# Performance work log

Measured on AMD Instinct MI355X. Metric: run time of the kernel, lower is better.

Reference implementation:

```python
import jax, jax.numpy as jnp
import numpy as np
from jax import lax

B, H, W = 256, 26, 4
LAT, QOUT = 64, 1024
K, D, Z = 4, 32, 64   # num_flows, num_ortho_vecs, z_size
STEPS = 100
BN_EPS = 1e-5


def setup_inputs():
    ks = iter(jax.random.split(jax.random.key(0), 80))
    def rn(shape, s=0.05):
        return jax.random.normal(next(ks), shape, jnp.float32) * s
    z1 = lambda n: jnp.zeros((n,), jnp.float32)
    o1 = lambda n: jnp.ones((n,), jnp.float32)
    return {
        "x": jax.random.normal(next(ks), (B, 1, H, W), jnp.float32),
        "eps": jax.random.normal(next(ks), (B, LAT), jnp.float32),
        "cw1": rn((32, 1, 3, 4)), "cb1": z1(32), "g1": o1(32), "be1": z1(32),
        "cw2": rn((16, 32, 5, 1)), "cb2": z1(16), "g2": o1(16), "be2": z1(16),
        "cw3": rn((8, 16, 7, 1)), "cb3": z1(8), "g3": o1(8), "be3": z1(8),
        "d1_w": rn((112, QOUT)), "d1_b": z1(QOUT), "bn1_g": o1(QOUT), "bn1_b": z1(QOUT),
        "mu_w": rn((QOUT, LAT)), "mu_b": z1(LAT),
        "lv_w": rn((QOUT, LAT)), "lv_b": z1(LAT),
        "ad_w": rn((QOUT, K * D * D)), "ad_b": z1(K * D * D),
        "adg1_w": rn((QOUT, K * D)), "adg1_b": z1(K * D),
        "adg2_w": rn((QOUT, K * D)), "adg2_b": z1(K * D),
        "aq_w": rn((QOUT, K * Z * D)), "aq_b": rn((K * Z * D,), 0.05),
        "ab_w": rn((QOUT, K * D)), "ab_b": z1(K * D),
        "d3_w": rn((LAT, QOUT)), "d3_b": z1(QOUT), "bn3_g": o1(QOUT), "bn3_b": z1(QOUT),
        "d4_w": rn((QOUT, 112)), "d4_b": z1(112), "bn4_g": o1(112), "bn4_b": z1(112),
        "tw1": rn((8, 16, 7, 1)), "tb1": z1(16), "tg1": o1(16), "tbe1": z1(16),
        "tw2": rn((16, 32, 5, 1)), "tb2": z1(32), "tg2": o1(32), "tbe2": z1(32),
        "tw3": rn((32, 1, 3, 4)), "tb3": z1(1),
    }


def _conv(x, w, b):
    y = lax.conv_general_dilated(x, w, (1, 1), 'VALID',
                                 dimension_numbers=('NCHW', 'OIHW', 'NCHW'))
    return y + b[None, :, None, None]


def _tconv(x, w, b):
    # torch ConvTranspose2d weight layout (in, out, kH, kW) == OIHW of the
    # forward conv being transposed -> transpose_kernel=True matches torch.
    y = lax.conv_transpose(x, w, (1, 1), 'VALID',
                           dimension_numbers=('NCHW', 'OIHW', 'NCHW'),
                           transpose_kernel=True)
    return y + b[None, :, None, None]


def _bn2d(x, g, b):  # BatchNorm2d, training mode (biased batch stats)
    m = x.mean((0, 2, 3), keepdims=True)
    v = ((x - m) ** 2).mean((0, 2, 3), keepdims=True)
    return (x - m) * lax.rsqrt(v + BN_EPS) * g[None, :, None, None] + b[None, :, None, None]


def _bn1d(x, g, b):  # BatchNorm1d, training mode
    m = x.mean(0)
    v = ((x - m) ** 2).mean(0)
    return (x - m) * lax.rsqrt(v + BN_EPS) * g + b


def reference(x, eps, cw1, cb1, g1, be1, cw2, cb2, g2, be2, cw3, cb3, g3, be3,
              d1_w, d1_b, bn1_g, bn1_b, mu_w, mu_b, lv_w, lv_b,
              ad_w, ad_b, adg1_w, adg1_b, adg2_w, adg2_b, aq_w, aq_b, ab_w, ab_b,
              d3_w, d3_b, bn3_g, bn3_b, d4_w, d4_b, bn4_g, bn4_b,
              tw1, tb1, tg1, tbe1, tw2, tb2, tg2, tbe2, tw3, tb3):
    # ---- encoder CNN ----
    h = jax.nn.relu(_bn2d(_conv(x, cw1, cb1), g1, be1))
    h = jax.nn.relu(_bn2d(_conv(h, cw2, cb2), g2, be2))
    h = jax.nn.relu(_bn2d(_conv(h, cw3, cb3), g3, be3))   # (B,8,14,1)
    out = h.reshape(B, -1)                                 # (B,112)
    out = jax.nn.relu(_bn1d(out @ d1_w + d1_b, bn1_g, bn1_b))
    mean = out @ mu_w + mu_b
    logvar = out @ lv_w + lv_b
    # ---- amortized flow parameters ----
    full_d = (out @ ad_w + ad_b).reshape(B, D, D, K)
    diag1 = jnp.tanh(out @ adg1_w + adg1_b).reshape(B, D, K)
    diag2 = jnp.tanh(out @ adg2_w + adg2_b).reshape(B, D, K)
    triu = jnp.triu(jnp.ones((D, D), x.dtype), 1)[None, :, :, None]
    di = jnp.arange(D)
    r1 = (full_d * triu).at[:, di, di, :].set(diag1)
    r2 = (jnp.transpose(full_d, (0, 2, 1, 3)) * triu).at[:, di, di, :].set(diag2)
    q = out @ aq_w + aq_b                                  # (B, K*Z*D)
    bflow = (out @ ab_w + ab_b).reshape(B, 1, D, K)
    # ---- Bjorck orthogonalization (100 fixed-point steps) ----
    qn = q.reshape(B * K, Z * D)
    qn = qn / jnp.linalg.norm(qn, axis=1, keepdims=True)
    amat = qn.reshape(B * K, Z, D)
    eye = jnp.eye(D, dtype=x.dtype)
    @jax.checkpoint
    def step(a, _):
        gram = jnp.einsum('nzd,nze->nde', a, a)            # a^T a, (N,D,D)
        a = jnp.einsum('nzd,nde->nze', a, eye + 0.5 * (eye - gram))
        return a, None
    amat, _ = lax.scan(step, amat, None, length=STEPS)
    q_ortho = amat.reshape(B, K, Z, D).transpose(1, 0, 2, 3)  # (K,B,Z,D)
    # ---- reparameterize + Sylvester flows ----
    z0 = mean + eps * jnp.exp(0.5 * logvar)
    z = z0
    ldj = jnp.zeros((B,), x.dtype)
    for k in range(K):
        r1k, r2k, qk, bk = r1[..., k], r2[..., k], q_ortho[k], bflow[..., k]
        qr2 = jnp.einsum('bzd,bed->bze', qk, r2k)          # q @ r2^T (B,Z,D)
        qr1 = jnp.einsum('bzd,bde->bze', qk, r1k)          # q @ r1   (B,Z,D)
        r2qzb = jnp.einsum('bz,bzd->bd', z, qr2)[:, None, :] + bk  # (B,1,D)
        z = jnp.einsum('bod,bzd->boz', jnp.tanh(r2qzb), qr1)[:, 0, :] + z
        dr1 = r1k[:, di, di]
        dr2 = r2k[:, di, di]
        diag_j = (1.0 - jnp.tanh(r2qzb) ** 2)[:, 0, :] * (dr1 * dr2) + 1.0
        ldj = ldj + jnp.log(jnp.abs(diag_j)).sum(-1)
    # ---- decoder ----
    d = jax.nn.relu(_bn1d(z @ d3_w + d3_b, bn3_g, bn3_b))
    d = jax.nn.relu(_bn1d(d @ d4_w + d4_b, bn4_g, bn4_b))
    d = d.reshape(B, 8, 14, 1)
    d = jax.nn.relu(_bn2d(_tconv(d, tw1, tb1), tg1, tbe1))
    d = jax.nn.relu(_bn2d(_tconv(d, tw2, tb2), tg2, tbe2))
    x_dec = _tconv(d, tw3, tb3)
    return (x_dec, mean, logvar, ldj, z0, z)
```

## Files before the change

kernel.cpp:

```cpp
#include <hip/hip_runtime.h>
#include <math.h>

#define NS_STEPS 30

typedef __attribute__((ext_vector_type(8))) _Float16 half8;
typedef __attribute__((ext_vector_type(4))) _Float16 half4v;
typedef __attribute__((ext_vector_type(8))) short short8;
typedef __attribute__((ext_vector_type(4))) float floatx4;

static __device__ inline unsigned short f2bf(float f) {
  union { float f; unsigned u; } v; v.f = f;
  unsigned r = v.u + 0x7fffu + ((v.u >> 16) & 1u);
  return (unsigned short)(r >> 16);
}
static __device__ inline float bf2f(unsigned short h) {
  union { unsigned u; float f; } v; v.u = ((unsigned)h) << 16;
  return v.f;
}

__global__ __launch_bounds__(256) void conv1_k(const float* __restrict__ x,
    const float* __restrict__ w, const float* __restrict__ bias,
    float* __restrict__ out) {
  __shared__ float ws[384];
  int tid = threadIdx.x;
  for (int i = tid; i < 384; i += 256) ws[i] = w[i];
  __syncthreads();
  int idx = blockIdx.x * 256 + tid;
  if (idx >= 196608) return;
  int b = idx / 768, r = idx % 768;
  int c = r / 24, h = r % 24;
  const float* xb = x + b * 104 + h * 4;
  const float* wc = ws + c * 12;
  float acc = bias[c];
  #pragma unroll
  for (int kh = 0; kh < 3; kh++) {
    #pragma unroll
    for (int kw = 0; kw < 4; kw++)
      acc += xb[kh * 4 + kw] * wc[kh * 4 + kw];
  }
  out[idx] = acc;
}

__global__ __launch_bounds__(256) void conv2_k(const float* __restrict__ in,
    const float* __restrict__ w, const float* __restrict__ bias,
    float* __restrict__ out) {
  __shared__ float ws[2560];
  int tid = threadIdx.x;
  for (int i = tid; i < 2560; i += 256) ws[i] = w[i];
  __syncthreads();
  int idx = blockIdx.x * 256 + tid;
  if (idx >= 81920) return;
  int b = idx / 320, r = idx % 320;
  int c = r / 20, h = r % 20;
  const float* ib = in + b * 768 + h;
  const float* wc = ws + c * 160;
  float acc = bias[c];
  for (int i = 0; i < 32; i++) {
    #pragma unroll
    for (int kh = 0; kh < 5; kh++)
      acc += ib[i * 24 + kh] * wc[i * 5 + kh];
  }
  out[idx] = acc;
}

__global__ __launch_bounds__(256) void conv3_k(const float* __restrict__ in,
    const float* __restrict__ w, const float* __restrict__ bias,
    float* __restrict__ out) {
  __shared__ float ws[896];
  int tid = threadIdx.x;
  for (int i = tid; i < 896; i += 256) ws[i] = w[i];
  __syncthreads();
  int idx = blockIdx.x * 256 + tid;
  if (idx >= 28672) return;
  int b = idx / 112, r = idx % 112;
  int c = r / 14, h = r % 14;
  const float* ib = in + b * 320 + h;
  const float* wc = ws + c * 112;
  float acc = bias[c];
  for (int i = 0; i < 16; i++) {
    #pragma unroll
    for (int kh = 0; kh < 7; kh++)
      acc += ib[i * 20 + kh] * wc[i * 7 + kh];
  }
  out[idx] = acc;
}

__global__ __launch_bounds__(256) void tconv1_k(const float* __restrict__ in,
    const float* __restrict__ w, const float* __restrict__ bias,
    float* __restrict__ out) {
  __shared__ float ws[896];
  int tid = threadIdx.x;
  for (int i = tid; i < 896; i += 256) ws[i] = w[i];
  __syncthreads();
  int idx = blockIdx.x * 256 + tid;
  if (idx >= 81920) return;
  int b = idx / 320, r = idx % 320;
  int c = r / 20, s = r % 20;
  float acc = bias[c];
  for (int o = 0; o < 8; o++) {
    #pragma unroll
    for (int kh = 0; kh < 7; kh++) {
      int hs = s - kh;
      if (hs >= 0 && hs < 14)
        acc += in[b * 112 + o * 14 + hs] * ws[o * 112 + c * 7 + kh];
    }
  }
  out[idx] = acc;
}

__global__ __launch_bounds__(256) void tconv2_k(const float* __restrict__ in,
    const float* __restrict__ w, const float* __restrict__ bias,
    float* __restrict__ out) {
  __shared__ float ws[2560];
  int tid = threadIdx.x;
  for (int i = tid; i < 2560; i += 256) ws[i] = w[i];
  __syncthreads();
  int idx = blockIdx.x * 256 + tid;
  if (idx >= 196608) return;
  int b = idx / 768, r = idx % 768;
  int c = r / 24, s = r % 24;
  float acc = bias[c];
  for (int o = 0; o < 16; o++) {
    #pragma unroll
    for (int kh = 0; kh < 5; kh++) {
      int hs = s - kh;
      if (hs >= 0 && hs < 20)
        acc += in[b * 320 + o * 20 + hs] * ws[o * 160 + c * 5 + kh];
    }
  }
  out[idx] = acc;
}

__global__ __launch_bounds__(256) void tconv3_k(const float* __restrict__ in,
    const float* __restrict__ w, const float* __restrict__ bias,
    float* __restrict__ out) {
  __shared__ float ws[384];
  int tid = threadIdx.x;
  for (int i = tid; i < 384; i += 256) ws[i] = w[i];
  __syncthreads();
  int idx = blockIdx.x * 256 + tid;
  if (idx >= 26624) return;
  int b = idx / 104, r = idx % 104;
  int sh = r / 4, sw = r % 4;
  float acc = bias[0];
  for (int o = 0; o < 32; o++) {
    #pragma unroll
    for (int kh = 0; kh < 3; kh++) {
      int hs = sh - kh;
      if (hs >= 0 && hs < 24)
        acc += in[b * 768 + o * 24 + hs] * ws[o * 12 + kh * 4 + sw];
    }
  }
  out[idx] = acc;
}

__global__ __launch_bounds__(256) void bn2d_k(float* __restrict__ x,
    const float* __restrict__ g, const float* __restrict__ be,
    int C, int HW) {
  __shared__ float rs[256], rs2[256];
  int c = blockIdx.x, tid = threadIdx.x;
  int total = 256 * HW;
  float s = 0.f, s2 = 0.f;
  for (int i = tid; i < total; i += 256) {
    int b = i / HW, j = i - b * HW;
    float v = x[(b * C + c) * HW + j];
    s += v; s2 += v * v;
  }
  rs[tid] = s; rs2[tid] = s2;
  __syncthreads();
  for (int off = 128; off > 0; off >>= 1) {
    if (tid < off) { rs[tid] += rs[tid + off]; rs2[tid] += rs2[tid + off]; }
    __syncthreads();
  }
  float m = rs[0] / (float)total;
  float var = rs2[0] / (float)total - m * m;
  float rstd = rsqrtf(var + 1e-5f) * g[c];
  float bb = be[c];
  for (int i = tid; i < total; i += 256) {
    int b = i / HW, j = i - b * HW;
    size_t idx = (size_t)(b * C + c) * HW + j;
    float v = (x[idx] - m) * rstd + bb;
    x[idx] = v > 0.f ? v : 0.f;
  }
}

__global__ __launch_bounds__(256) void bn1d_k(float* __restrict__ x,
    const float* __restrict__ g, const float* __restrict__ be, int N) {
  __shared__ float p1[8][32], p2[8][32];
  int t = threadIdx.x;
  int cl = t & 31, rg = t >> 5;
  int c = blockIdx.x * 32 + cl;
  float s = 0.f, s2 = 0.f;
  if (c < N) {
    for (int r = rg * 32; r < rg * 32 + 32; r++) {
      float v = x[r * N + c];
      s += v; s2 += v * v;
    }
  }
  p1[rg][cl] = s; p2[rg][cl] = s2;
  __syncthreads();
  float ts = 0.f, ts2 = 0.f;
  #pragma unroll
  for (int i = 0; i < 8; i++) { ts += p1[i][cl]; ts2 += p2[i][cl]; }
  float m = ts * (1.f / 256.f);
  float var = ts2 * (1.f / 256.f) - m * m;
  float rstd = rsqrtf(var + 1e-5f) * ((c < N) ? g[c] : 1.f);
  float bb = (c < N) ? be[c] : 0.f;
  if (c < N) {
    for (int r = rg * 32; r < rg * 32 + 32; r++) {
      float v = (x[r * N + c] - m) * rstd + bb;
      x[r * N + c] = v > 0.f ? v : 0.f;
    }
  }
}

__global__ __launch_bounds__(256) void gemm_os_k(const float* __restrict__ A,
    const float* __restrict__ W, const float* __restrict__ bias,
    float* __restrict__ C, int K, int N) {
  __shared__ float As[112 * 68];
  __shared__ float Bs[112 * 68];
  int tid = threadIdx.x;
  int nb = blockIdx.x, mb = blockIdx.y;
  int K16 = K >> 4;
  {
    int row = tid >> 2;
    const float* Ar = A + (size_t)(mb * 64 + row) * K;
    for (int i = 0; i < K16; i++) {
      int j = (tid & 3) + 4 * i;
      float4 v = *(const float4*)(Ar + j * 4);
      int k = j * 4;
      As[k * 68 + row] = v.x;
      As[(k + 1) * 68 + row] = v.y;
      As[(k + 2) * 68 + row] = v.z;
      As[(k + 3) * 68 + row] = v.w;
    }
  }
  {
    int n4 = (tid & 15) * 4;
    for (int i = 0; i < K16; i++) {
      int k = (tid >> 4) + 16 * i;
      float4 v = *(const float4*)(W + (size_t)k * N + nb * 64 + n4);
      *(float4*)(Bs + k * 68 + n4) = v;
    }
  }
  __syncthreads();
  int tm = tid >> 4, tn = tid & 15;
  int m0 = tm * 4, n0 = tn * 4;
  float acc[4][4] = {{0.f}};
  #pragma unroll 8
  for (int kk = 0; kk < K; kk++) {
    float4 a = *(const float4*)(As + kk * 68 + m0);
    float4 b = *(const float4*)(Bs + kk * 68 + n0);
    acc[0][0] += a.x*b.x; acc[0][1] += a.x*b.y; acc[0][2] += a.x*b.z; acc[0][3] += a.x*b.w;
    acc[1][0] += a.y*b.x; acc[1][1] += a.y*b.y; acc[1][2] += a.y*b.z; acc[1][3] += a.y*b.w;
    acc[2][0] += a.z*b.x; acc[2][1] += a.z*b.y; acc[2][2] += a.z*b.z; acc[2][3] += a.z*b.w;
    acc[3][0] += a.w*b.x; acc[3][1] += a.w*b.y; acc[3][2] += a.w*b.z; acc[3][3] += a.w*b.w;
  }
  #pragma unroll
  for (int i = 0; i < 4; i++) {
    int m = mb * 64 + m0 + i;
    #pragma unroll
    for (int j = 0; j < 4; j++) {
      int n = nb * 64 + n0 + j;
      C[(size_t)m * N + n] = acc[i][j] + bias[n];
    }
  }
}

__global__ __launch_bounds__(256) void gemm_ks_k(const float* __restrict__ A,
    const float* __restrict__ W, const float* __restrict__ bias,
    float* __restrict__ C) {
  __shared__ float As[64 * 68];
  __shared__ float Bs[64 * 68];
  int tid = threadIdx.x;
  int nb = blockIdx.x, mb = blockIdx.y, kc = blockIdx.z;
  int k0 = kc * 64;
  {
    int row = tid >> 2;
    const float* Ar = A + (size_t)(mb * 64 + row) * 1024 + k0;
    #pragma unroll
    for (int i = 0; i < 4; i++) {
      int j = (tid & 3) + 4 * i;
      float4 v = *(const float4*)(Ar + j * 4);
      int k = j * 4;
      As[k * 68 + row] = v.x;
      As[(k + 1) * 68 + row] = v.y;
      As[(k + 2) * 68 + row] = v.z;
      As[(k + 3) * 68 + row] = v.w;
    }
  }
  {
    int n4 = (tid & 15) * 4;
    int nbase = nb * 64 + n4;
    #pragma unroll
    for (int i = 0; i < 4; i++) {
      int k = (tid >> 4) + 16 * i;
      const float* Wr = W + (size_t)(k0 + k) * 112;
      float4 v;
      v.x = (nbase     < 112) ? Wr[nbase]     : 0.f;
      v.y = (nbase + 1 < 112) ? Wr[nbase + 1] : 0.f;
      v.z = (nbase + 2 < 112) ? Wr[nbase + 2] : 0.f;
      v.w = (nbase + 3 < 112) ? Wr[nbase + 3] : 0.f;
      *(float4*)(Bs + k * 68 + n4) = v;
    }
  }
  __syncthreads();
  int tm = tid >> 4, tn = tid & 15;
  int m0 = tm * 4, n0 = tn * 4;
  float acc[4][4] = {{0.f}};
  #pragma unroll 8
  for (int kk = 0; kk < 64; kk++) {
    float4 a = *(const float4*)(As + kk * 68 + m0);
    float4 b = *(const float4*)(Bs + kk * 68 + n0);
    acc[0][0] += a.x*b.x; acc[0][1] += a.x*b.y; acc[0][2] += a.x*b.z; acc[0][3] += a.x*b.w;
    acc[1][0] += a.y*b.x; acc[1][1] += a.y*b.y; acc[1][2] += a.y*b.z; acc[1][3] += a.y*b.w;
    acc[2][0] += a.z*b.x; acc[2][1] += a.z*b.y; acc[2][2] += a.z*b.z; acc[2][3] += a.z*b.w;
    acc[3][0] += a.w*b.x; acc[3][1] += a.w*b.y; acc[3][2] += a.w*b.z; acc[3][3] += a.w*b.w;
  }
  #pragma unroll
  for (int i = 0; i < 4; i++) {
    int m = mb * 64 + m0 + i;
    #pragma unroll
    for (int j = 0; j < 4; j++) {
      int n = nb * 64 + n0 + j;
      if (n < 112) {
        float v = acc[i][j] + (kc == 0 ? bias[n] : 0.f);
        atomicAdd(&C[m * 112 + n], v);
      }
    }
  }
}

__global__ __launch_bounds__(256) void prep_a_k(const float* __restrict__ A,
    short* __restrict__ ahi, short* __restrict__ alo) {
  int gi = blockIdx.x * 256 + threadIdx.x;
  int lane = gi & 63;
  int t = gi >> 6;
  int mt = t & 3; t >>= 2;
  int c = t & 31; int mb = t >> 5;
  int row = mb * 64 + mt * 16 + (lane & 15);
  int k0 = c * 32 + (lane >> 4) * 8;
  const float* src = A + (size_t)row * 1024 + k0;
  float4 v0 = *(const float4*)(src);
  float4 v1 = *(const float4*)(src + 4);
  float av[8] = {v0.x, v0.y, v0.z, v0.w, v1.x, v1.y, v1.z, v1.w};
  short8 h, lo;
  #pragma unroll
  for (int i = 0; i < 8; i++) {
    unsigned short hh = f2bf(av[i]);
    h[i] = (short)hh;
    lo[i] = (short)f2bf(av[i] - bf2f(hh));
  }
  *(short8*)(ahi + (size_t)gi * 8) = h;
  *(short8*)(alo + (size_t)gi * 8) = lo;
}

struct HeadArgs {
  const float* W[7];
  const float* b[7];
  float* dst[7];
  int off[8];
  int ldw[7];
  int op[7];
};

__global__ __launch_bounds__(256) void heads_mfma_k(const short* __restrict__ ahi,
                                                    const short* __restrict__ alo,
                                                    HeadArgs ha) {
  __shared__ __align__(16) short Wsh[2][2][2048];
  int tid = threadIdx.x;
  int nb = blockIdx.x, mb = blockIdx.y;
  int r = 0;
  int gc = nb * 64;
  while (gc >= ha.off[r + 1]) r++;
  const float* Wp = ha.W[r];
  const float* bias = ha.b[r];
  float* dst = ha.dst[r];
  int ldw = ha.ldw[r];
  int op = ha.op[r];
  int nloc0 = gc - ha.off[r];

  int w = tid >> 6, l = tid & 63;
  int lane16 = l & 15, quad = l >> 4;

  int c64 = tid & 63, q4 = tid >> 6;
  const float* wcol = Wp + (size_t)q4 * 8 * ldw + nloc0 + c64;
  int wg = ((c64 >> 4) * 64 + q4 * 16 + (c64 & 15)) * 8;

  const short* agh = ahi + (size_t)mb * 65536;
  const short* agl = alo + (size_t)mb * 65536;

  const floatx4 zero4 = {0.f, 0.f, 0.f, 0.f};
  floatx4 acc[4] = {zero4, zero4, zero4, zero4};

  float wreg[8];
  short8 whi, wlo;

  #pragma unroll
  for (int j = 0; j < 8; j++) wreg[j] = wcol[(size_t)j * ldw];
  #pragma unroll
  for (int j = 0; j < 8; j++) {
    unsigned short hh = f2bf(wreg[j]);
    whi[j] = (short)hh;
    wlo[j] = (short)f2bf(wreg[j] - bf2f(hh));
  }
  *(short8*)(&Wsh[0][0][wg]) = whi;
  *(short8*)(&Wsh[0][1][wg]) = wlo;
  #pragma unroll
  for (int j = 0; j < 8; j++) wreg[j] = wcol[(size_t)(32 + j) * ldw];
  __syncthreads();
  #pragma unroll
  for (int j = 0; j < 8; j++) {
    unsigned short hh = f2bf(wreg[j]);
    whi[j] = (short)hh;
    wlo[j] = (short)f2bf(wreg[j] - bf2f(hh));
  }

  for (int ch = 0; ch < 32; ++ch) {
    int p = ch & 1;
    if (ch < 31) {
      *(short8*)(&Wsh[p ^ 1][0][wg]) = whi;
      *(short8*)(&Wsh[p ^ 1][1][wg]) = wlo;
    }
    if (ch < 30) {
      #pragma unroll
      for (int j = 0; j < 8; j++)
        wreg[j] = wcol[(size_t)((ch + 2) * 32 + j) * ldw];
    }
    short8 bh = *(const short8*)(&Wsh[p][0][(w * 64 + l) * 8]);
    short8 bl = *(const short8*)(&Wsh[p][1][(w * 64 + l) * 8]);
    short8 ah[4], al4[4];
    #pragma unroll
    for (int mt = 0; mt < 4; mt++) {
      size_t ao = (size_t)ch * 2048 + mt * 512 + l * 8;
      ah[mt]  = *(const short8*)(agh + ao);
      al4[mt] = *(const short8*)(agl + ao);
    }
    #pragma unroll
    for (int mt = 0; mt < 4; mt++) {
      acc[mt] = __builtin_amdgcn_mfma_f32_16x16x32_bf16(ah[mt], bh, acc[mt], 0, 0, 0);
      acc[mt] = __builtin_amdgcn_mfma_f32_16x16x32_bf16(ah[mt], bl, acc[mt], 0, 0, 0);
      acc[mt] = __builtin_amdgcn_mfma_f32_16x16x32_bf16(al4[mt], bh, acc[mt], 0, 0, 0);
    }
    if (ch < 30) {
      #pragma unroll
      for (int j = 0; j < 8; j++) {
        unsigned short hh = f2bf(wreg[j]);
        whi[j] = (short)hh;
        wlo[j] = (short)f2bf(wreg[j] - bf2f(hh));
      }
    }
    __syncthreads();
  }

  int n = nloc0 + w * 16 + lane16;
  float bv = bias[n];
  #pragma unroll
  for (int mt = 0; mt < 4; mt++) {
    #pragma unroll
    for (int i = 0; i < 4; i++) {
      int m = mb * 64 + mt * 16 + quad * 4 + i;
      float v = acc[mt][i] + bv;
      if (op == 1) v = tanhf(v);
      dst[(size_t)m * ldw + n] = v;
    }
  }
}

__global__ __launch_bounds__(64) void ns_f16split_k(const float* __restrict__ q,
                                                    float* __restrict__ amat) {
  __align__(16) __shared__ _Float16 arena[12288];
  int l = threadIdx.x;
  int lane16 = l & 15, quad = l >> 4;
  _Float16* Ah_cm = arena;
  _Float16* Al_cm = arena + 2304;
  _Float16* Mh_cm = arena + 4608;
  _Float16* Ml_cm = arena + 5888;
  _Float16* Ah_rm = arena + 7168;
  _Float16* Al_rm = arena + 9728;
  float* Afin = (float*)arena;

  const float* g = q + (size_t)blockIdx.x * 2048;
  float* o = amat + (size_t)blockIdx.x * 2048;

  float vals[32];
  float ss = 0.f;
  #pragma unroll
  for (int j = 0; j < 8; j++) {
    float4 v = *(const float4*)(g + l * 32 + j * 4);
    vals[4*j] = v.x; vals[4*j+1] = v.y; vals[4*j+2] = v.z; vals[4*j+3] = v.w;
    ss += v.x*v.x + v.y*v.y + v.z*v.z + v.w*v.w;
  }
  #pragma unroll
  for (int off = 32; off > 0; off >>= 1) ss += __shfl_xor(ss, off);
  float rn = rsqrtf(ss);
  #pragma unroll
  for (int i = 0; i < 32; i++) vals[i] *= rn;
  #pragma unroll
  for (int j = 0; j < 8; j++) {
    half4v ph, pl;
    #pragma unroll
    for (int r = 0; r < 4; r++) {
      float v = vals[4*j + r];
      _Float16 h = (_Float16)v;
      _Float16 lo = (_Float16)(v - (float)h);
      ph[r] = h; pl[r] = lo;
    }
    *(half4v*)(Ah_rm + l * 40 + j * 4) = ph;
    *(half4v*)(Al_rm + l * 40 + j * 4) = pl;
  }
  #pragma unroll
  for (int i = 0; i < 32; i++) {
    float v = vals[i];
    _Float16 h = (_Float16)v;
    Ah_cm[i * 72 + l] = h;
    Al_cm[i * 72 + l] = (_Float16)(v - (float)h);
  }
  __syncthreads();

  const floatx4 zero4 = {0.f, 0.f, 0.f, 0.f};
  for (int s = 0; s < NS_STEPS; s++) {
    bool last = (s == NS_STEPS - 1);
    half8 fah[2][2], fal[2][2];
    #pragma unroll
    for (int ti = 0; ti < 2; ti++)
      #pragma unroll
      for (int c = 0; c < 2; c++) {
        fah[ti][c] = *(half8*)(Ah_cm + (ti * 16 + lane16) * 72 + c * 32 + quad * 8);
        fal[ti][c] = *(half8*)(Al_cm + (ti * 16 + lane16) * 72 + c * 32 + quad * 8);
      }
    floatx4 gf[2][2] = {{zero4, zero4}, {zero4, zero4}};
    #pragma unroll
    for (int ti = 0; ti < 2; ti++)
      #pragma unroll
      for (int tj = 0; tj < 2; tj++)
        #pragma unroll
        for (int c = 0; c < 2; c++) {
          gf[ti][tj] = __builtin_amdgcn_mfma_f32_16x16x32_f16(
              fah[ti][c], fah[tj][c], gf[ti][tj], 0, 0, 0);
          gf[ti][tj] = __builtin_amdgcn_mfma_f32_16x16x32_f16(
              fah[ti][c], fal[tj][c], gf[ti][tj], 0, 0, 0);
          gf[ti][tj] = __builtin_amdgcn_mfma_f32_16x16x32_f16(
              fal[ti][c], fah[tj][c], gf[ti][tj], 0, 0, 0);
        }
    #pragma unroll
    for (int ti = 0; ti < 2; ti++)
      #pragma unroll
      for (int tj = 0; tj < 2; tj++) {
        int col = tj * 16 + lane16;
        int row0 = ti * 16 + quad * 4;
        half4v ph, pl;
        #pragma unroll
        for (int r = 0; r < 4; r++) {
          float m = ((row0 + r) == col ? 1.5f : 0.f) - 0.5f * gf[ti][tj][r];
          _Float16 h = (_Float16)m;
          ph[r] = h; pl[r] = (_Float16)(m - (float)h);
        }
        *(half4v*)(Mh_cm + col * 40 + row0) = ph;
        *(half4v*)(Ml_cm + col * 40 + row0) = pl;
      }
    __syncthreads();
    half8 fmh[2], fml[2], fbh[4], fbl[4];
    #pragma unroll
    for (int ti = 0; ti < 2; ti++) {
      fmh[ti] = *(half8*)(Mh_cm + (ti * 16 + lane16) * 40 + quad * 8);
      fml[ti] = *(half8*)(Ml_cm + (ti * 16 + lane16) * 40 + quad * 8);
    }
    #pragma unroll
    for (int tj = 0; tj < 4; tj++) {
      fbh[tj] = *(half8*)(Ah_rm + (tj * 16 + lane16) * 40 + quad * 8);
      fbl[tj] = *(half8*)(Al_rm + (tj * 16 + lane16) * 40 + quad * 8);
    }
    floatx4 df[2][4];
    #pragma unroll
    for (int ti = 0; ti < 2; ti++)
      #pragma unroll
      for (int tj = 0; tj < 4; tj++) {
        df[ti][tj] = __builtin_amdgcn_mfma_f32_16x16x32_f16(
            fmh[ti], fbh[tj], zero4, 0, 0, 0);
        df[ti][tj] = __builtin_amdgcn_mfma_f32_16x16x32_f16(
            fmh[ti], fbl[tj], df[ti][tj], 0, 0, 0);
        df[ti][tj] = __builtin_amdgcn_mfma_f32_16x16x32_f16(
            fml[ti], fbh[tj], df[ti][tj], 0, 0, 0);
      }
    __syncthreads();
    if (!last) {
      #pragma unroll
      for (int ti = 0; ti < 2; ti++)
        #pragma unroll
        for (int tj = 0; tj < 4; tj++) {
          int z = tj * 16 + lane16;
          int d0 = ti * 16 + quad * 4;
          half4v ph, pl;
          #pragma unroll
          for (int r = 0; r < 4; r++) {
            float v = df[ti][tj][r];
            _Float16 h = (_Float16)v;
            ph[r] = h; pl[r] = (_Float16)(v - (float)h);
          }
          *(half4v*)(Ah_rm + z * 40 + d0) = ph;
          *(half4v*)(Al_rm + z * 40 + d0) = pl;
          #pragma unroll
          for (int r = 0; r < 4; r++) {
            Ah_cm[(d0 + r) * 72 + z] = ph[r];
            Al_cm[(d0 + r) * 72 + z] = pl[r];
          }
        }
    } else {
      #pragma unroll
      for (int ti = 0; ti < 2; ti++)
        #pragma unroll
        for (int tj = 0; tj < 4; tj++) {
          int z = tj * 16 + lane16;
          int d0 = ti * 16 + quad * 4;
          float4 v;
          v.x = df[ti][tj][0]; v.y = df[ti][tj][1];
          v.z = df[ti][tj][2]; v.w = df[ti][tj][3];
          *(float4*)(Afin + z * 36 + d0) = v;
        }
    }
    __syncthreads();
  }
  #pragma unroll
  for (int j = 0; j < 8; j++) {
    int f = j * 256 + l * 4;
    int z = f >> 5, d = f & 31;
    float4 v = *(const float4*)(Afin + z * 36 + d);
    *(float4*)(o + f) = v;
  }
}

__global__ __launch_bounds__(64) void flow_k(const float* __restrict__ amat,
    const float* __restrict__ fd, const float* __restrict__ dg1,
    const float* __restrict__ dg2, const float* __restrict__ ab,
    const float* __restrict__ eps, float* __restrict__ dout) {
  __shared__ float Ps[32][64];
  __shared__ float wsh[32], tsh[32], ush[32];
  int b = blockIdx.x, l = threadIdx.x;
  float mv  = dout[26624 + b * 64 + l];
  float lvv = dout[43008 + b * 64 + l];
  float z0 = mv + eps[b * 64 + l] * expf(0.5f * lvv);
  dout[59648 + b * 64 + l] = z0;
  float zv = z0;
  float ldj = 0.f;
  float q[32];
  for (int k = 0; k < 4; k++) {
    const float4* qrow = (const float4*)(amat + (size_t)(b * 4 + k) * 2048 + l * 32);
    #pragma unroll
    for (int j = 0; j < 8; j++) {
      float4 v = qrow[j];
      q[4*j] = v.x; q[4*j+1] = v.y; q[4*j+2] = v.z; q[4*j+3] = v.w;
    }
    #pragma unroll
    for (int d = 0; d < 32; d++) Ps[d][l] = zv * q[d];
    __syncthreads();
    if (l < 32) {
      const float4* pr = (const float4*)Ps[l];
      float s = 0.f;
      #pragma unroll
      for (int j = 0; j < 16; j++) {
        float4 v = pr[j];
        s += v.x + v.y + v.z + v.w;
      }
      wsh[l] = s;
    }
    __syncthreads();
    if (l < 32) {
      int e = l;
      float acc = ab[b * 128 + e * 4 + k] + wsh[e] * dg2[b * 128 + e * 4 + k];
      for (int d = e + 1; d < 32; d++)
        acc += wsh[d] * fd[b * 4096 + d * 128 + e * 4 + k];
      float tt = tanhf(acc);
      tsh[e] = tt;
      float dd = (1.f - tt * tt) * (dg1[b*128 + e*4 + k] * dg2[b*128 + e*4 + k]) + 1.f;
      ldj += logf(fabsf(dd));
    }
    __syncthreads();
    if (l < 32) {
      int d = l;
      float acc = tsh[d] * dg1[b * 128 + d * 4 + k];
      for (int e = d + 1; e < 32; e++)
        acc += fd[b * 4096 + d * 128 + e * 4 + k] * tsh[e];
      ush[d] = acc;
    }
    __syncthreads();
    #pragma unroll
    for (int d = 0; d < 32; d++) zv += q[d] * ush[d];
    __syncthreads();
  }
  dout[76032 + b * 64 + l] = zv;
  for (int off = 16; off > 0; off >>= 1) ldj += __shfl_down(ldj, off, 32);
  if (l == 0) dout[59392 + b] = ldj;
}

extern "C" void kernel_launch(void* const* d_in, const int* in_sizes, int n_in,
                              void* d_out, int out_size, void* d_ws, size_t ws_size,
                              hipStream_t stream) {
  (void)in_sizes; (void)n_in; (void)out_size; (void)ws_size;
  const float* x     = (const float*)d_in[0];
  const float* eps   = (const float*)d_in[1];
  const float* cw1   = (const float*)d_in[2];
  const float* cb1   = (const float*)d_in[3];
  const float* g1    = (const float*)d_in[4];
  const float* be1   = (const float*)d_in[5];
  const float* cw2   = (const float*)d_in[6];
  const float* cb2   = (const float*)d_in[7];
  const float* g2    = (const float*)d_in[8];
  const float* be2   = (const float*)d_in[9];
  const float* cw3   = (const float*)d_in[10];
  const float* cb3   = (const float*)d_in[11];
  const float* g3    = (const float*)d_in[12];
  const float* be3   = (const float*)d_in[13];
  const float* d1_w  = (const float*)d_in[14];
  const float* d1_b  = (const float*)d_in[15];
  const float* bn1_g = (const float*)d_in[16];
  const float* bn1_b = (const float*)d_in[17];
  const float* mu_w  = (const float*)d_in[18];
  const float* mu_b  = (const float*)d_in[19];
  const float* lv_w  = (const float*)d_in[20];
  const float* lv_b  = (const float*)d_in[21];
  const float* ad_w  = (const float*)d_in[22];
  const float* ad_b  = (const float*)d_in[23];
  const float* adg1_w= (const float*)d_in[24];
  const float* adg1_b= (const float*)d_in[25];
  const float* adg2_w= (const float*)d_in[26];
  const float* adg2_b= (const float*)d_in[27];
  const float* aq_w  = (const float*)d_in[28];
  const float* aq_b  = (const float*)d_in[29];
  const float* ab_w  = (const float*)d_in[30];
  const float* ab_b  = (const float*)d_in[31];
  const float* d3_w  = (const float*)d_in[32];
  const float* d3_b  = (const float*)d_in[33];
  const float* bn3_g = (const float*)d_in[34];
  const float* bn3_b = (const float*)d_in[35];
  const float* d4_w  = (const float*)d_in[36];
  const float* d4_b  = (const float*)d_in[37];
  const float* bn4_g = (const float*)d_in[38];
  const float* bn4_b = (const float*)d_in[39];
  const float* tw1   = (const float*)d_in[40];
  const float* tb1   = (const float*)d_in[41];
  const float* tg1   = (const float*)d_in[42];
  const float* tbe1  = (const float*)d_in[43];
  const float* tw2   = (const float*)d_in[44];
  const float* tb2   = (const float*)d_in[45];
  const float* tg2   = (const float*)d_in[46];
  const float* tbe2  = (const float*)d_in[47];
  const float* tw3   = (const float*)d_in[48];
  const float* tb3   = (const float*)d_in[49];

  float* out = (float*)d_out;
  float* wsf = (float*)d_ws;
  float* h1   = wsf;
  float* h2   = wsf + 196608;
  float* h3   = wsf + 278528;
  float* out1 = wsf + 307200;
  float* fd   = wsf + 569344;
  float* dg1  = wsf + 1617920;
  float* dg2  = wsf + 1650688;
  float* qb   = wsf + 1683456;
  float* ab   = wsf + 3780608;
  float* amat = wsf + 3813376;
  float* dec1 = out1;
  float* dec2 = h3;
  float* t1   = h2;
  float* t2   = h1;

  short* ahi = (short*)wsf;
  short* alo = ahi + 262144;

  float* mean_o = out + 26624;
  float* lv_o   = out + 43008;
  float* z_o    = out + 76032;

  conv1_k<<<768, 256, 0, stream>>>(x, cw1, cb1, h1);
  bn2d_k<<<32, 256, 0, stream>>>(h1, g1, be1, 32, 24);
  conv2_k<<<320, 256, 0, stream>>>(h1, cw2, cb2, h2);
  bn2d_k<<<16, 256, 0, stream>>>(h2, g2, be2, 16, 20);
  conv3_k<<<112, 256, 0, stream>>>(h2, cw3, cb3, h3);
  bn2d_k<<<8, 256, 0, stream>>>(h3, g3, be3, 8, 14);

  gemm_os_k<<<dim3(16, 4), 256, 0, stream>>>(h3, d1_w, d1_b, out1, 112, 1024);
  bn1d_k<<<32, 256, 0, stream>>>(out1, bn1_g, bn1_b, 1024);

  prep_a_k<<<128, 256, 0, stream>>>(out1, ahi, alo);

  HeadArgs ha;
  ha.W[0] = mu_w;   ha.b[0] = mu_b;   ha.dst[0] = mean_o; ha.ldw[0] = 64;   ha.op[0] = 0;
  ha.W[1] = lv_w;   ha.b[1] = lv_b;   ha.dst[1] = lv_o;   ha.ldw[1] = 64;   ha.op[1] = 0;
  ha.W[2] = ad_w;   ha.b[2] = ad_b;   ha.dst[2] = fd;     ha.ldw[2] = 4096; ha.op[2] = 0;
  ha.W[3] = adg1_w; ha.b[3] = adg1_b; ha.dst[3] = dg1;    ha.ldw[3] = 128;  ha.op[3] = 1;
  ha.W[4] = adg2_w; ha.b[4] = adg2_b; ha.dst[4] = dg2;    ha.ldw[4] = 128;  ha.op[4] = 1;
  ha.W[5] = aq_w;   ha.b[5] = aq_b;   ha.dst[5] = qb;     ha.ldw[5] = 8192; ha.op[5] = 0;
  ha.W[6] = ab_w;   ha.b[6] = ab_b;   ha.dst[6] = ab;     ha.ldw[6] = 128;  ha.op[6] = 0;
  ha.off[0] = 0;    ha.off[1] = 64;   ha.off[2] = 128;  ha.off[3] = 4224;
  ha.off[4] = 4352; ha.off[5] = 4480; ha.off[6] = 12672; ha.off[7] = 12800;
  heads_mfma_k<<<dim3(200, 4), 256, 0, stream>>>(ahi, alo, ha);

  ns_f16split_k<<<1024, 64, 0, stream>>>(qb, amat);
  flow_k<<<256, 64, 0, stream>>>(amat, fd, dg1, dg2, ab, eps, out);

  gemm_os_k<<<dim3(16, 4), 256, 0, stream>>>(z_o, d3_w, d3_b, dec1, 64, 1024);
  bn1d_k<<<32, 256, 0, stream>>>(dec1, bn3_g, bn3_b, 1024);
  hipMemsetAsync(dec2, 0, 28672 * sizeof(float), stream);
  gemm_ks_k<<<dim3(2, 4, 16), 256, 0, stream>>>(dec1, d4_w, d4_b, dec2);
  bn1d_k<<<4, 256, 0, stream>>>(dec2, bn4_g, bn4_b, 112);

  tconv1_k<<<320, 256, 0, stream>>>(dec2, tw1, tb1, t1);
  bn2d_k<<<16, 256, 0, stream>>>(t1, tg1, tbe1, 16, 20);
  tconv2_k<<<768, 256, 0, stream>>>(t1, tw2, tb2, t2);
  bn2d_k<<<32, 256, 0, stream>>>(t2, tg2, tbe2, 32, 24);
  tconv3_k<<<104, 256, 0, stream>>>(t2, tw3, tb3, out);
}
```

Measured before the change: 521.2 us.

## Retile heads GEMM so each block covers all rows and reuses weight tiles

The heads GEMM grid drops the M-dimension blocks, so each 64-column block now computes all 256 rows, with each wave owning 64 rows and all four 16-column N fragments. Each weight chunk is converted to bf16 hi/lo and staged in LDS once per column block rather than four times, and A-fragments are register double-buffered one chunk ahead. The aim is to cut the redundant weight loads and conversions, which are the main global traffic. In exchange the grid shrinks from 800 to 200 blocks and each thread holds 16 accumulators plus prefetch buffers, which lowers occupancy and may leave CUs idle.

```diff
diff --git a/kernel.cpp b/kernel.cpp
--- a/kernel.cpp
+++ b/kernel.cpp
@@ -369,7 +369,7 @@
                                                     HeadArgs ha) {
   __shared__ __align__(16) short Wsh[2][2][2048];
   int tid = threadIdx.x;
-  int nb = blockIdx.x, mb = blockIdx.y;
+  int nb = blockIdx.x;
   int r = 0;
   int gc = nb * 64;
   while (gc >= ha.off[r + 1]) r++;
@@ -387,14 +387,19 @@
   const float* wcol = Wp + (size_t)q4 * 8 * ldw + nloc0 + c64;
   int wg = ((c64 >> 4) * 64 + q4 * 16 + (c64 & 15)) * 8;
 
-  const short* agh = ahi + (size_t)mb * 65536;
-  const short* agl = alo + (size_t)mb * 65536;
+  const short* agh = ahi + (size_t)w * 65536;
+  const short* agl = alo + (size_t)w * 65536;
 
   const floatx4 zero4 = {0.f, 0.f, 0.f, 0.f};
-  floatx4 acc[4] = {zero4, zero4, zero4, zero4};
+  floatx4 acc[4][4];
+  #pragma unroll
+  for (int mt = 0; mt < 4; mt++)
+    #pragma unroll
+    for (int nf = 0; nf < 4; nf++) acc[mt][nf] = zero4;
 
   float wreg[8];
   short8 whi, wlo;
+  short8 aCh[4], aCl[4], aNh[4], aNl[4];
 
   #pragma unroll
   for (int j = 0; j < 8; j++) wreg[j] = wcol[(size_t)j * ldw];
@@ -408,6 +413,12 @@
   *(short8*)(&Wsh[0][1][wg]) = wlo;
   #pragma unroll
   for (int j = 0; j < 8; j++) wreg[j] = wcol[(size_t)(32 + j) * ldw];
+  #pragma unroll
+  for (int mt = 0; mt < 4; mt++) {
+    size_t ao = (size_t)mt * 512 + l * 8;
+    aCh[mt] = *(const short8*)(agh + ao);
+    aCl[mt] = *(const short8*)(agl + ao);
+  }
   __syncthreads();
   #pragma unroll
   for (int j = 0; j < 8; j++) {
@@ -416,6 +427,7 @@
     wlo[j] = (short)f2bf(wreg[j] - bf2f(hh));
   }
 
+  #pragma unroll 2
   for (int ch = 0; ch < 32; ++ch) {
     int p = ch & 1;
     if (ch < 31) {
@@ -427,21 +439,28 @@
       for (int j = 0; j < 8; j++)
         wreg[j] = wcol[(size_t)((ch + 2) * 32 + j) * ldw];
     }
-    short8 bh = *(const short8*)(&Wsh[p][0][(w * 64 + l) * 8]);
-    short8 bl = *(const short8*)(&Wsh[p][1][(w * 64 + l) * 8]);
-    short8 ah[4], al4[4];
-    #pragma unroll
-    for (int mt = 0; mt < 4; mt++) {
-      size_t ao = (size_t)ch * 2048 + mt * 512 + l * 8;
-      ah[mt]  = *(const short8*)(agh + ao);
-      al4[mt] = *(const short8*)(agl + ao);
-    }
-    #pragma unroll
-    for (int mt = 0; mt < 4; mt++) {
-      acc[mt] = __builtin_amdgcn_mfma_f32_16x16x32_bf16(ah[mt], bh, acc[mt], 0, 0, 0);
-      acc[mt] = __builtin_amdgcn_mfma_f32_16x16x32_bf16(ah[mt], bl, acc[mt], 0, 0, 0);
-      acc[mt] = __builtin_amdgcn_mfma_f32_16x16x32_bf16(al4[mt], bh, acc[mt], 0, 0, 0);
-    }
+    if (ch < 31) {
+      #pragma unroll
+      for (int mt = 0; mt < 4; mt++) {
+        size_t ao = (size_t)((ch + 1) * 4 + mt) * 512 + l * 8;
+        aNh[mt] = *(const short8*)(agh + ao);
+        aNl[mt] = *(const short8*)(agl + ao);
+      }
+    }
+    short8 bh[4], bl[4];
+    #pragma unroll
+    for (int nf = 0; nf < 4; nf++) {
+      bh[nf] = *(const short8*)(&Wsh[p][0][(nf * 64 + l) * 8]);
+      bl[nf] = *(const short8*)(&Wsh[p][1][(nf * 64 + l) * 8]);
+    }
+    #pragma unroll
+    for (int mt = 0; mt < 4; mt++)
+      #pragma unroll
+      for (int nf = 0; nf < 4; nf++) {
+        acc[mt][nf] = __builtin_amdgcn_mfma_f32_16x16x32_bf16(aCh[mt], bh[nf], acc[mt][nf], 0, 0, 0);
+        acc[mt][nf] = __builtin_amdgcn_mfma_f32_16x16x32_bf16(aCh[mt], bl[nf], acc[mt][nf], 0, 0, 0);
+        acc[mt][nf] = __builtin_amdgcn_mfma_f32_16x16x32_bf16(aCl[mt], bh[nf], acc[mt][nf], 0, 0, 0);
+      }
     if (ch < 30) {
       #pragma unroll
       for (int j = 0; j < 8; j++) {
@@ -450,19 +469,26 @@
         wlo[j] = (short)f2bf(wreg[j] - bf2f(hh));
       }
     }
-    __syncthreads();
-  }
-
-  int n = nloc0 + w * 16 + lane16;
-  float bv = bias[n];
-  #pragma unroll
-  for (int mt = 0; mt < 4; mt++) {
-    #pragma unroll
-    for (int i = 0; i < 4; i++) {
-      int m = mb * 64 + mt * 16 + quad * 4 + i;
-      float v = acc[mt][i] + bv;
-      if (op == 1) v = tanhf(v);
-      dst[(size_t)m * ldw + n] = v;
+    if (ch < 31) {
+      #pragma unroll
+      for (int mt = 0; mt < 4; mt++) { aCh[mt] = aNh[mt]; aCl[mt] = aNl[mt]; }
+    }
+    __syncthreads();
+  }
+
+  #pragma unroll
+  for (int nf = 0; nf < 4; nf++) {
+    int n = nloc0 + nf * 16 + lane16;
+    float bv = bias[n];
+    #pragma unroll
+    for (int mt = 0; mt < 4; mt++) {
+      #pragma unroll
+      for (int i = 0; i < 4; i++) {
+        int m = w * 64 + mt * 16 + quad * 4 + i;
+        float v = acc[mt][nf][i] + bv;
+        if (op == 1) v = tanhf(v);
+        dst[(size_t)m * ldw + n] = v;
+      }
     }
   }
 }
@@ -794,7 +820,7 @@
   ha.W[6] = ab_w;   ha.b[6] = ab_b;   ha.dst[6] = ab;     ha.ldw[6] = 128;  ha.op[6] = 0;
   ha.off[0] = 0;    ha.off[1] = 64;   ha.off[2] = 128;  ha.off[3] = 4224;
   ha.off[4] = 4352; ha.off[5] = 4480; ha.off[6] = 12672; ha.off[7] = 12800;
-  heads_mfma_k<<<dim3(200, 4), 256, 0, stream>>>(ahi, alo, ha);
+  heads_mfma_k<<<dim3(200), 256, 0, stream>>>(ahi, alo, ha);
 
   ns_f16split_k<<<1024, 64, 0, stream>>>(qb, amat);
   flow_k<<<256, 64, 0, stream>>>(amat, fd, dg1, dg2, ab, eps, out);
```

Result: no change. 521.8 us (+0.1%).
